# Performance work log

Hardware: AMD Instinct MI355X
Metric: run time of the kernel (lower is better)

The kernel has to match this reference:

```python
import jax, jax.numpy as jnp
import numpy as np

EMBED = 1024
HEADS = 16
HEAD_DIM = EMBED // HEADS
N, SEQ = 8, 1024


def setup_inputs() -> dict:
    key = jax.random.key(0)
    ks = jax.random.split(key, 8)
    s = 1.0 / np.sqrt(HEAD_DIM)
    so = 1.0 / np.sqrt(EMBED)
    return {
        "values": jax.random.normal(ks[0], (N, SEQ, EMBED), jnp.float32),
        "keys": jax.random.normal(ks[1], (N, SEQ, EMBED), jnp.float32),
        "query": jax.random.normal(ks[2], (N, SEQ, EMBED), jnp.float32),
        "mask": jnp.ones((N, 1, 1, SEQ), jnp.int32),
        "Wv": jax.random.normal(ks[3], (HEAD_DIM, HEAD_DIM), jnp.float32) * s,
        "Wk": jax.random.normal(ks[4], (HEAD_DIM, HEAD_DIM), jnp.float32) * s,
        "Wq": jax.random.normal(ks[5], (HEAD_DIM, HEAD_DIM), jnp.float32) * s,
        "Wo": jax.random.normal(ks[6], (EMBED, EMBED), jnp.float32) * so,
        "bo": jnp.zeros((EMBED,), jnp.float32),
    }


def reference(values, keys, query, mask, Wv, Wk, Wq, Wo, bo):
    n, ql = query.shape[0], query.shape[1]
    # split heads: (N, L, H, D)
    v = values.reshape(n, -1, HEADS, HEAD_DIM)
    k = keys.reshape(n, -1, HEADS, HEAD_DIM)
    q = query.reshape(n, -1, HEADS, HEAD_DIM)
    # per-head linear projections (nn.Linear, no bias): x @ W^T
    v = jnp.einsum("nlhd,ed->nlhe", v, Wv)
    k = jnp.einsum("nlhd,ed->nlhe", k, Wk)
    q = jnp.einsum("nlhd,ed->nlhe", q, Wq)
    # scores: (N, H, Q, K)
    energy = jnp.einsum("nqhd,nkhd->nhqk", q, k)
    energy = jnp.where(mask == 0, jnp.float32(-1e10), energy)
    attn = jax.nn.softmax(energy / jnp.sqrt(jnp.float32(EMBED)), axis=-1)
    out = jnp.einsum("nhqk,nkhd->nqhd", attn, v).reshape(n, ql, EMBED)
    return out @ Wo.T + bo
```

## Files before the change

### kernel.cpp

```cpp
#include <hip/hip_runtime.h>
#include <hip/hip_bf16.h>
#include <stdint.h>

typedef unsigned short u16;
typedef __bf16 bf16_t;
typedef bf16_t bf16x8 __attribute__((ext_vector_type(8)));
typedef float f32x4 __attribute__((ext_vector_type(4)));
typedef float f32x16 __attribute__((ext_vector_type(16)));

#define MFMA16(a, b, c) __builtin_amdgcn_mfma_f32_16x16x32_bf16((a), (b), (c), 0, 0, 0)
#define MFMA32(a, b, c) __builtin_amdgcn_mfma_f32_32x32x16_bf16((a), (b), (c), 0, 0, 0)

#define NBATCH 8
#define SEQL 1024
#define EMB 1024
#define NHEAD 16
#define HD 64

static __device__ __forceinline__ u16 f2b(float f) {
  bf16_t b = (bf16_t)f;
  return __builtin_bit_cast(u16, b);
}

union V16 { uint4 u; bf16x8 b; };

static __device__ __forceinline__ bf16x8 ldb8(const u16* p) {
  V16 v; v.u = *(const uint4*)p; return v.b;
}

static __device__ __forceinline__ bf16x8 cvt8(const float* p) {
  float4 a = *(const float4*)p;
  float4 b = *(const float4*)(p + 4);
  bf16x8 r;
  r[0] = (bf16_t)a.x; r[1] = (bf16_t)a.y; r[2] = (bf16_t)a.z; r[3] = (bf16_t)a.w;
  r[4] = (bf16_t)b.x; r[5] = (bf16_t)b.y; r[6] = (bf16_t)b.z; r[7] = (bf16_t)b.w;
  return r;
}

static __device__ __forceinline__ void gload16(const void* g, void* l) {
  __builtin_amdgcn_global_load_lds((__attribute__((address_space(1))) void*)(uintptr_t)g,
                                   (__attribute__((address_space(3))) void*)l, 16, 0, 0);
}

static __device__ __forceinline__ unsigned cvtpk(float lo, float hi) {
  unsigned r;
  asm("v_cvt_pk_bf16_f32 %0, %1, %2" : "=v"(r) : "v"(lo), "v"(hi));
  return r;
}

static __device__ __forceinline__ f32x16 zero16() {
  f32x16 z;
#pragma unroll
  for (int i = 0; i < 16; ++i) z[i] = 0.f;
  return z;
}

__global__ __launch_bounds__(256) void k_proj3(const float* __restrict__ Xv, const float* __restrict__ Xk,
                                               const float* __restrict__ Xq, const float* __restrict__ Wv,
                                               const float* __restrict__ Wk, const float* __restrict__ Wq,
                                               u16* __restrict__ Vt, u16* __restrict__ Kp, u16* __restrict__ Qp,
                                               const float* __restrict__ Wo, u16* __restrict__ Wob) {
  int z = blockIdx.z;
  if (z == 3) {
    size_t i = ((size_t)blockIdx.x * 256 + threadIdx.x) * 8;
    V16 v; v.b = cvt8(Wo + i);
    *(uint4*)(Wob + i) = v.u;
    return;
  }
  __shared__ __align__(16) u16 xs[16 * 1024];
  __shared__ __align__(16) u16 obuf[4][16 * 72];
  __shared__ __align__(16) u16 ob2[4][1024];
  const float* X = (z == 0) ? Xv : (z == 1) ? Xk : Xq;
  const float* W = (z == 0) ? Wv : (z == 1) ? Wk : Wq;
  u16* Out = (z == 0) ? Vt : (z == 1) ? Kp : Qp;
  int vmode = (z == 0);
  float qs = (z == 2) ? 0.04508422f : 1.0f;

  int gr0 = blockIdx.x * 16;
  int n = gr0 >> 10, l0 = gr0 & 1023;
  int tid = threadIdx.x, w = tid >> 6, lane = tid & 63;
  int lr = lane & 15, lg = lane >> 4;

  bf16x8 bw[4][2];
#pragma unroll
  for (int c = 0; c < 4; ++c)
#pragma unroll
    for (int kk = 0; kk < 2; ++kk)
      bw[c][kk] = cvt8(W + (lr + 16 * c) * HD + kk * 32 + lg * 8);

#pragma unroll
  for (int i = 0; i < 8; ++i) {
    int m = i * 256 + tid;
    int row = m >> 7, cc = m & 127;
    V16 v; v.b = cvt8(X + (size_t)gr0 * 1024 + (size_t)m * 8);
    *(uint4*)(xs + row * 1024 + ((cc ^ (row & 7)) * 8)) = v.u;
  }
  __syncthreads();

#pragma unroll 1
  for (int h4 = 0; h4 < 4; ++h4) {
    int h = w * 4 + h4;
    int nh = n * 16 + h;
    bf16x8 a0 = ldb8(xs + lr * 1024 + (((h * 8 + 0 + lg) ^ (lr & 7)) * 8));
    bf16x8 a1 = ldb8(xs + lr * 1024 + (((h * 8 + 4 + lg) ^ (lr & 7)) * 8));
    f32x4 acc[4];
#pragma unroll
    for (int c = 0; c < 4; ++c) {
      f32x4 zz = {0.f, 0.f, 0.f, 0.f};
      zz = MFMA16(a0, bw[c][0], zz);
      zz = MFMA16(a1, bw[c][1], zz);
      acc[c] = zz;
    }
    if (!vmode) {
      u16* ob = obuf[w];
#pragma unroll
      for (int c = 0; c < 4; ++c)
#pragma unroll
        for (int rr = 0; rr < 4; ++rr)
          ob[(lg * 4 + rr) * 72 + lr + 16 * c] = f2b(acc[c][rr] * qs);
      int orow = lane >> 2, oseg = lane & 3;
      uint4 v0 = *(const uint4*)(ob + orow * 72 + oseg * 16);
      uint4 v1 = *(const uint4*)(ob + orow * 72 + oseg * 16 + 8);
      u16* dst = Out + ((size_t)nh * SEQL + l0 + orow) * HD + oseg * 16;
      *(uint4*)dst = v0;
      *(uint4*)(dst + 8) = v1;
    } else {
      u16* o2 = ob2[w];
#pragma unroll
      for (int c = 0; c < 4; ++c) {
        ushort4 p;
        p.x = f2b(acc[c][0]); p.y = f2b(acc[c][1]); p.z = f2b(acc[c][2]); p.w = f2b(acc[c][3]);
        *(ushort4*)(o2 + (lg >> 1) * 512 + (lr + 16 * c) * 8 + (lg & 1) * 4) = p;
      }
      int lb0 = l0 >> 3;
#pragma unroll
      for (int lbi = 0; lbi < 2; ++lbi) {
        uint4 vv = *(const uint4*)(o2 + lbi * 512 + lane * 8);
        *(uint4*)(Out + (size_t)nh * 65536 + (size_t)(lb0 + lbi) * 512 + lane * 8) = vv;
      }
    }
  }
}

__global__ __launch_bounds__(256, 2) void k_attn2(const u16* __restrict__ Qp, const u16* __restrict__ Kp,
                                                  const u16* __restrict__ Vt, const int* __restrict__ mask,
                                                  u16* __restrict__ AO) {
  __shared__ __align__(16) u16 SMEM[2][8192];
  __shared__ unsigned long long mkb[16];
  __shared__ __align__(16) float winv[4][2][32];

  int nh = blockIdx.x;
  int n = nh >> 4, h = nh & 15;
  int tid = threadIdx.x, w = tid >> 6, lane = tid & 63;
  int q = lane & 31, hi = lane >> 5;
  int q0w = blockIdx.y * 256 + w * 64;

  bf16x8 bq[2][4];
#pragma unroll
  for (int g = 0; g < 2; ++g) {
    const u16* qbase = Qp + ((size_t)nh * SEQL + q0w + g * 32 + q) * HD + hi * 8;
#pragma unroll
    for (int kk = 0; kk < 4; ++kk) bq[g][kk] = ldb8(qbase + kk * 16);
  }

  const u16* gK = Kp + (size_t)nh * SEQL * HD;
  const u16* gV = Vt + (size_t)nh * HD * SEQL;
  int sr = lane >> 3, sslot = lane & 7;

  auto STAGE = [&](int b, int t) {
#pragma unroll
    for (int j = 0; j < 2; ++j) {
      int r = 16 * w + 8 * j + sr;
      int slot = sslot ^ (r & 7);
      gload16(gK + ((size_t)(t * 64 + r)) * HD + slot * 8,
              &SMEM[b][w * 1024 + j * 512]);
      gload16(gV + (size_t)(t * 8 + slot) * 512 + r * 8,
              &SMEM[b][4096 + w * 1024 + j * 512]);
    }
  };

  STAGE(0, 0);
#pragma unroll 1
  for (int t = w; t < 16; t += 4) {
    int mv = mask[n * SEQL + t * 64 + lane];
    unsigned long long b = __ballot(mv != 0);
    if (lane == 0) mkb[t] = b;
  }
  __syncthreads();

  f32x16 oacc[2][2];
  oacc[0][0] = zero16(); oacc[0][1] = zero16();
  oacc[1][0] = zero16(); oacc[1][1] = zero16();
  float lsum0 = 0.f, lsum1 = 0.f;
  int buf = 0;

#pragma unroll 1
  for (int kt = 0; kt < 16; ++kt) {
    if (kt < 15) STAGE(buf ^ 1, kt + 1);
    const u16* KB = &SMEM[buf][0];
    const u16* VB = &SMEM[buf][4096];
    unsigned long long mb = mkb[kt];

#pragma unroll
    for (int c = 0; c < 2; ++c) {
      f32x16 s0 = zero16(), s1 = zero16();
      {
        int row = 32 * c + q;
        int swz = (row & 7) << 3;
        const u16* kr = KB + row * 64;
        __builtin_amdgcn_s_setprio(1);
#pragma unroll
        for (int kk = 0; kk < 4; ++kk) {
          bf16x8 ak = ldb8(kr + ((16 * kk + 8 * hi) ^ swz));
          s0 = MFMA32(ak, bq[0][kk], s0);
          s1 = MFMA32(ak, bq[1][kk], s1);
        }
        __builtin_amdgcn_s_setprio(0);
      }

#pragma unroll
      for (int rr = 0; rr < 16; ++rr) {
        s0[rr] = __builtin_amdgcn_exp2f(s0[rr]);
        s1[rr] = __builtin_amdgcn_exp2f(s1[rr]);
      }
      if (mb != ~0ull) {
#pragma unroll
        for (int rr = 0; rr < 16; ++rr) {
          int kpos = 32 * c + 4 * hi + (rr & 3) + 8 * (rr >> 2);
          if (!((mb >> kpos) & 1)) { s0[rr] = 0.f; s1[rr] = 0.f; }
        }
      }
#pragma unroll
      for (int rr = 0; rr < 16; ++rr) { lsum0 += s0[rr]; lsum1 += s1[rr]; }

      bf16x8 pa0[2], pa1[2];
#pragma unroll
      for (int p2 = 0; p2 < 2; ++p2) {
        unsigned a0 = cvtpk(s0[8 * p2 + 0], s0[8 * p2 + 1]);
        unsigned a1 = cvtpk(s0[8 * p2 + 2], s0[8 * p2 + 3]);
        unsigned b0 = cvtpk(s0[8 * p2 + 4], s0[8 * p2 + 5]);
        unsigned b1 = cvtpk(s0[8 * p2 + 6], s0[8 * p2 + 7]);
        auto r0 = __builtin_amdgcn_permlane32_swap(a0, b0, false, false);
        auto r1 = __builtin_amdgcn_permlane32_swap(a1, b1, false, false);
        union { unsigned u[4]; bf16x8 v; } pu;
        pu.u[0] = r0[0]; pu.u[1] = r1[0]; pu.u[2] = r0[1]; pu.u[3] = r1[1];
        pa0[p2] = pu.v;
        unsigned c0 = cvtpk(s1[8 * p2 + 0], s1[8 * p2 + 1]);
        unsigned c1 = cvtpk(s1[8 * p2 + 2], s1[8 * p2 + 3]);
        unsigned d0 = cvtpk(s1[8 * p2 + 4], s1[8 * p2 + 5]);
        unsigned d1 = cvtpk(s1[8 * p2 + 6], s1[8 * p2 + 7]);
        auto r2 = __builtin_amdgcn_permlane32_swap(c0, d0, false, false);
        auto r3 = __builtin_amdgcn_permlane32_swap(c1, d1, false, false);
        union { unsigned u[4]; bf16x8 v; } pv;
        pv.u[0] = r2[0]; pv.u[1] = r3[0]; pv.u[2] = r2[1]; pv.u[3] = r3[1];
        pa1[p2] = pv.v;
      }

      __builtin_amdgcn_s_setprio(1);
#pragma unroll
      for (int cp = 0; cp < 2; ++cp) {
        int row = 32 * cp + q;
        int swz = (row & 7) << 3;
        const u16* vr = VB + row * 64;
#pragma unroll
        for (int p2 = 0; p2 < 2; ++p2) {
          int tq = 2 * c + p2;
          bf16x8 vb = ldb8(vr + ((16 * tq + 8 * hi) ^ swz));
          oacc[0][cp] = MFMA32(pa0[p2], vb, oacc[0][cp]);
          oacc[1][cp] = MFMA32(pa1[p2], vb, oacc[1][cp]);
        }
      }
      __builtin_amdgcn_s_setprio(0);
    }
    __syncthreads();
    buf ^= 1;
  }

  float t0 = lsum0 + __shfl_xor(lsum0, 32);
  float t1 = lsum1 + __shfl_xor(lsum1, 32);
  if (!hi) { winv[w][0][q] = 1.0f / t0; winv[w][1][q] = 1.0f / t1; }

  u16* ob = &SMEM[0][0] + w * 2560;
  int orow = lane >> 1, ohalf = lane & 1;
#pragma unroll
  for (int g = 0; g < 2; ++g) {
    float iq[16];
#pragma unroll
    for (int w2 = 0; w2 < 4; ++w2) {
      float4 f = *(const float4*)&winv[w][g][8 * w2 + 4 * hi];
      iq[4 * w2 + 0] = f.x; iq[4 * w2 + 1] = f.y; iq[4 * w2 + 2] = f.z; iq[4 * w2 + 3] = f.w;
    }
#pragma unroll
    for (int cp = 0; cp < 2; ++cp)
#pragma unroll
      for (int rr = 0; rr < 16; ++rr) {
        int qr = (rr & 3) + 8 * (rr >> 2) + 4 * hi;
        ob[qr * 80 + 32 * cp + q] = f2b(oacc[g][cp][rr] * iq[rr]);
      }
    __builtin_amdgcn_s_barrier();
    const u16* srcp = ob + orow * 80 + ohalf * 32;
    uint4 v0 = *(const uint4*)srcp;
    uint4 v1 = *(const uint4*)(srcp + 8);
    uint4 v2 = *(const uint4*)(srcp + 16);
    uint4 v3 = *(const uint4*)(srcp + 24);
    u16* dst = AO + ((size_t)(n * SEQL + q0w + g * 32 + orow)) * EMB + h * HD + ohalf * 32;
    *(uint4*)dst = v0;
    *(uint4*)(dst + 8) = v1;
    *(uint4*)(dst + 16) = v2;
    *(uint4*)(dst + 24) = v3;
  }
}

__global__ __launch_bounds__(256) void k_out(const u16* __restrict__ AO, const u16* __restrict__ Wob,
                                             const float* __restrict__ bo, float* __restrict__ Y) {
  __shared__ __align__(16) u16 As[2][8192];
  __shared__ __align__(16) u16 Bs[2][8192];
  int g = blockIdx.x;
  int xcd = g & 7, rr_ = g >> 3;
  int m0 = (xcd * 8 + (rr_ >> 3)) * 128;
  int n0 = (rr_ & 7) * 128;
  int tid = threadIdx.x, w = tid >> 6, lane = tid & 63;
  int lr = lane & 15, lg = lane >> 4;
  int wr = w >> 1, wc = w & 1;
  int sr8 = lane >> 3, ss8 = lane & 7;

  auto STAGE = [&](int b, int kb) {
#pragma unroll
    for (int j = 0; j < 4; ++j) {
      int row = 32 * w + 8 * j + sr8;
      gload16(AO + (size_t)(m0 + row) * EMB + kb * 64 + ((ss8 ^ (row & 7)) * 8),
              &As[b][w * 2048 + j * 512]);
      gload16(Wob + (size_t)(n0 + row) * EMB + kb * 64 + ((ss8 ^ (row & 7)) * 8),
              &Bs[b][w * 2048 + j * 512]);
    }
  };

  f32x4 acc[4][4] = {};
  STAGE(0, 0);
  __syncthreads();
  int buf = 0;
#pragma unroll 1
  for (int kb = 0; kb < 16; ++kb) {
    if (kb < 15) STAGE(buf ^ 1, kb + 1);
    bf16x8 a0[4], a1[4], b0[4], b1[4];
#pragma unroll
    for (int mi = 0; mi < 4; ++mi) {
      int row = wr * 64 + mi * 16 + lr;
      a0[mi] = ldb8(&As[buf][row * 64 + (((0 + lg) ^ (row & 7)) * 8)]);
      a1[mi] = ldb8(&As[buf][row * 64 + (((4 + lg) ^ (row & 7)) * 8)]);
    }
#pragma unroll
    for (int ni = 0; ni < 4; ++ni) {
      int row = wc * 64 + ni * 16 + lr;
      b0[ni] = ldb8(&Bs[buf][row * 64 + (((0 + lg) ^ (row & 7)) * 8)]);
      b1[ni] = ldb8(&Bs[buf][row * 64 + (((4 + lg) ^ (row & 7)) * 8)]);
    }
    __builtin_amdgcn_s_setprio(1);
#pragma unroll
    for (int mi = 0; mi < 4; ++mi)
#pragma unroll
      for (int ni = 0; ni < 4; ++ni) {
        acc[mi][ni] = MFMA16(a0[mi], b0[ni], acc[mi][ni]);
        acc[mi][ni] = MFMA16(a1[mi], b1[ni], acc[mi][ni]);
      }
    __builtin_amdgcn_s_setprio(0);
    __syncthreads();
    buf ^= 1;
  }
#pragma unroll
  for (int ni = 0; ni < 4; ++ni) {
    float bov = bo[n0 + wc * 64 + ni * 16 + lr];
#pragma unroll
    for (int mi = 0; mi < 4; ++mi) {
#pragma unroll
      for (int rr = 0; rr < 4; ++rr) {
        int row = m0 + wr * 64 + mi * 16 + lg * 4 + rr;
        int col = n0 + wc * 64 + ni * 16 + lr;
        Y[(size_t)row * EMB + col] = acc[mi][ni][rr] + bov;
      }
    }
  }
}

extern "C" void kernel_launch(void* const* d_in, const int* in_sizes, int n_in,
                              void* d_out, int out_size, void* d_ws, size_t ws_size,
                              hipStream_t stream) {
  (void)in_sizes; (void)n_in; (void)out_size; (void)ws_size;
  const float* values = (const float*)d_in[0];
  const float* keys   = (const float*)d_in[1];
  const float* query  = (const float*)d_in[2];
  const int*   mask   = (const int*)d_in[3];
  const float* Wv = (const float*)d_in[4];
  const float* Wk = (const float*)d_in[5];
  const float* Wq = (const float*)d_in[6];
  const float* Wo = (const float*)d_in[7];
  const float* bo = (const float*)d_in[8];
  float* out = (float*)d_out;

  u16* ws  = (u16*)d_ws;
  u16* Qp  = ws;
  u16* Kp  = ws + (size_t)8 * 1024 * 1024;
  u16* Vt  = ws + (size_t)16 * 1024 * 1024;
  u16* AO  = ws + (size_t)24 * 1024 * 1024;
  u16* Wob = ws + (size_t)32 * 1024 * 1024;

  k_proj3<<<dim3(512, 1, 4), dim3(256), 0, stream>>>(values, keys, query, Wv, Wk, Wq, Vt, Kp, Qp, Wo, Wob);
  k_attn2<<<dim3(128, 4), dim3(256), 0, stream>>>(Qp, Kp, Vt, mask, AO);
  k_out<<<dim3(512), dim3(256), 0, stream>>>(AO, Wob, bo, out);
}
```

Baseline: 97.65 us.

## Split attention key range in two and merge partial outputs

Attention is split along the key dimension into two halves via a third grid dimension. Each half writes an unnormalized bf16 partial output and its row denominators to workspace, and a new merge kernel adds the partials and normalizes. This doubles the block count to expose more parallelism and shorten each block's serial key loop. In exchange it adds an extra kernel launch, extra global traffic for partial outputs and denominators, and rounds the unnormalized partials to bf16 before merging.

```diff
diff --git a/kernel.cpp b/kernel.cpp
--- a/kernel.cpp
+++ b/kernel.cpp
@@ -144,13 +144,15 @@
 
 __global__ __launch_bounds__(256, 2) void k_attn2(const u16* __restrict__ Qp, const u16* __restrict__ Kp,
                                                   const u16* __restrict__ Vt, const int* __restrict__ mask,
-                                                  u16* __restrict__ AO) {
+                                                  u16* __restrict__ AO, u16* __restrict__ Op1,
+                                                  float* __restrict__ den0, float* __restrict__ den1) {
   __shared__ __align__(16) u16 SMEM[2][8192];
   __shared__ unsigned long long mkb[16];
-  __shared__ __align__(16) float winv[4][2][32];
 
   int nh = blockIdx.x;
   int n = nh >> 4, h = nh & 15;
+  int s = blockIdx.z;
+  int kt0 = s * 8;
   int tid = threadIdx.x, w = tid >> 6, lane = tid & 63;
   int q = lane & 31, hi = lane >> 5;
   int q0w = blockIdx.y * 256 + w * 64;
@@ -179,9 +181,9 @@
     }
   };
 
-  STAGE(0, 0);
+  STAGE(0, kt0);
 #pragma unroll 1
-  for (int t = w; t < 16; t += 4) {
+  for (int t = kt0 + w; t < kt0 + 8; t += 4) {
     int mv = mask[n * SEQL + t * 64 + lane];
     unsigned long long b = __ballot(mv != 0);
     if (lane == 0) mkb[t] = b;
@@ -195,8 +197,8 @@
   int buf = 0;
 
 #pragma unroll 1
-  for (int kt = 0; kt < 16; ++kt) {
-    if (kt < 15) STAGE(buf ^ 1, kt + 1);
+  for (int kt = kt0; kt < kt0 + 8; ++kt) {
+    if (kt < kt0 + 7) STAGE(buf ^ 1, kt + 1);
     const u16* KB = &SMEM[buf][0];
     const u16* VB = &SMEM[buf][4096];
     unsigned long long mb = mkb[kt];
@@ -276,26 +278,25 @@
     buf ^= 1;
   }
 
+  u16* Od = s ? Op1 : AO;
+  float* dd = s ? den1 : den0;
   float t0 = lsum0 + __shfl_xor(lsum0, 32);
   float t1 = lsum1 + __shfl_xor(lsum1, 32);
-  if (!hi) { winv[w][0][q] = 1.0f / t0; winv[w][1][q] = 1.0f / t1; }
+  if (!hi) {
+    dd[nh * 1024 + q0w + q] = t0;
+    dd[nh * 1024 + q0w + 32 + q] = t1;
+  }
 
   u16* ob = &SMEM[0][0] + w * 2560;
   int orow = lane >> 1, ohalf = lane & 1;
 #pragma unroll
   for (int g = 0; g < 2; ++g) {
-    float iq[16];
-#pragma unroll
-    for (int w2 = 0; w2 < 4; ++w2) {
-      float4 f = *(const float4*)&winv[w][g][8 * w2 + 4 * hi];
-      iq[4 * w2 + 0] = f.x; iq[4 * w2 + 1] = f.y; iq[4 * w2 + 2] = f.z; iq[4 * w2 + 3] = f.w;
-    }
 #pragma unroll
     for (int cp = 0; cp < 2; ++cp)
 #pragma unroll
       for (int rr = 0; rr < 16; ++rr) {
         int qr = (rr & 3) + 8 * (rr >> 2) + 4 * hi;
-        ob[qr * 80 + 32 * cp + q] = f2b(oacc[g][cp][rr] * iq[rr]);
+        ob[qr * 80 + 32 * cp + q] = f2b(oacc[g][cp][rr]);
       }
     __builtin_amdgcn_s_barrier();
     const u16* srcp = ob + orow * 80 + ohalf * 32;
@@ -303,12 +304,30 @@
     uint4 v1 = *(const uint4*)(srcp + 8);
     uint4 v2 = *(const uint4*)(srcp + 16);
     uint4 v3 = *(const uint4*)(srcp + 24);
-    u16* dst = AO + ((size_t)(n * SEQL + q0w + g * 32 + orow)) * EMB + h * HD + ohalf * 32;
+    u16* dst = Od + ((size_t)(n * SEQL + q0w + g * 32 + orow)) * EMB + h * HD + ohalf * 32;
     *(uint4*)dst = v0;
     *(uint4*)(dst + 8) = v1;
     *(uint4*)(dst + 16) = v2;
     *(uint4*)(dst + 24) = v3;
   }
+}
+
+__global__ __launch_bounds__(256) void k_merge(u16* __restrict__ AO, const u16* __restrict__ Op1,
+                                               const float* __restrict__ den0, const float* __restrict__ den1) {
+  size_t base = ((size_t)blockIdx.x * 256 + threadIdx.x) * 8;
+  int qlin = (int)(base >> 10);
+  int e = (int)(base & 1023);
+  int h = e >> 6;
+  int n = qlin >> 10, q = qlin & 1023;
+  int di = (n * 16 + h) * 1024 + q;
+  float inv = 1.0f / (den0[di] + den1[di]);
+  V16 a; a.u = *(const uint4*)(AO + base);
+  V16 b; b.u = *(const uint4*)(Op1 + base);
+  V16 o;
+#pragma unroll
+  for (int j = 0; j < 8; ++j)
+    o.b[j] = (bf16_t)(((float)a.b[j] + (float)b.b[j]) * inv);
+  *(uint4*)(AO + base) = o.u;
 }
 
 __global__ __launch_bounds__(256) void k_out(const u16* __restrict__ AO, const u16* __restrict__ Wob,
@@ -397,14 +416,18 @@
   const float* bo = (const float*)d_in[8];
   float* out = (float*)d_out;
 
-  u16* ws  = (u16*)d_ws;
-  u16* Qp  = ws;
-  u16* Kp  = ws + (size_t)8 * 1024 * 1024;
-  u16* Vt  = ws + (size_t)16 * 1024 * 1024;
-  u16* AO  = ws + (size_t)24 * 1024 * 1024;
-  u16* Wob = ws + (size_t)32 * 1024 * 1024;
+  u16* ws   = (u16*)d_ws;
+  u16* Qp   = ws;
+  u16* Kp   = ws + (size_t)8 * 1024 * 1024;
+  u16* Vt   = ws + (size_t)16 * 1024 * 1024;
+  u16* AO   = ws + (size_t)24 * 1024 * 1024;
+  u16* Wob  = ws + (size_t)32 * 1024 * 1024;
+  u16* Op1  = ws + (size_t)33 * 1024 * 1024;
+  float* den0 = (float*)(ws + (size_t)41 * 1024 * 1024);
+  float* den1 = (float*)(ws + (size_t)41 * 1024 * 1024 + 512 * 1024);
 
   k_proj3<<<dim3(512, 1, 4), dim3(256), 0, stream>>>(values, keys, query, Wv, Wk, Wq, Vt, Kp, Qp, Wo, Wob);
-  k_attn2<<<dim3(128, 4), dim3(256), 0, stream>>>(Qp, Kp, Vt, mask, AO);
+  k_attn2<<<dim3(128, 4, 2), dim3(256), 0, stream>>>(Qp, Kp, Vt, mask, AO, Op1, den0, den1);
+  k_merge<<<dim3(4096), dim3(256), 0, stream>>>(AO, Op1, den0, den1);
   k_out<<<dim3(512), dim3(256), 0, stream>>>(AO, Wob, bo, out);
 }
```

Result: slower. 113.6 us (+16.4%).
